# Performance work log

Hardware: AMD Instinct MI355X
Metric: run time of the kernel (lower is better)

The kernel has to match this reference:

```python
import jax, jax.numpy as jnp
import numpy as np

N_NODES = 100000
N_EDGES = 3200000
OUT_FEATURES = 128


def setup_inputs() -> dict:
    key = jax.random.key(0)
    k1, k2, k3, k4, k5 = jax.random.split(key, 5)
    edge_row = jax.random.randint(k1, (N_EDGES,), 0, N_NODES, dtype=jnp.int32)
    edge_col = jax.random.randint(k2, (N_EDGES,), 0, N_NODES, dtype=jnp.int32)
    edge_val = jax.random.uniform(k3, (N_EDGES,), dtype=jnp.float32)
    stdv = 1.0 / np.sqrt(OUT_FEATURES)
    weight = jax.random.uniform(k4, (N_NODES, OUT_FEATURES), minval=-stdv, maxval=stdv, dtype=jnp.float32)
    bias = jax.random.uniform(k5, (OUT_FEATURES,), minval=-stdv, maxval=stdv, dtype=jnp.float32)
    return {"edge_row": edge_row, "edge_col": edge_col, "edge_val": edge_val,
            "weight": weight, "bias": bias}


def reference(edge_row, edge_col, edge_val, weight, bias):
    # SpMM: out = adj @ weight, adj given in COO (row, col, val), shape [N, N]
    n_nodes = weight.shape[0]
    gathered = edge_val[:, None] * weight[edge_col]            # [E, F]
    out = jax.ops.segment_sum(gathered, edge_row, num_segments=n_nodes)  # [N, F]
    return out + bias
```

## Files before the change

kernel.cpp:

```cpp
#include <hip/hip_runtime.h>

#define F 128
#define RB 64
#define RB_SHIFT 6
#define CAP 4096
#define SCH 4096
#define PT3 512
#define EPT3 (SCH / PT3)
#define NSEG 8
#define COL_BITS 17
#define COL_MASK 0x1FFFF
#define MAXNB 2048

__global__ __launch_bounds__(256) void cvt_kernel(const float2* __restrict__ w2,
                                                  ushort* __restrict__ wq,
                                                  float* __restrict__ scales,
                                                  int n_nodes) {
    int row = blockIdx.x * 4 + (threadIdx.x >> 6);
    if (row >= n_nodes) return;
    int lane = threadIdx.x & 63;
    float2 f = w2[(size_t)row * 64 + lane];
    float m = fmaxf(fabsf(f.x), fabsf(f.y));
    for (int off = 32; off; off >>= 1) m = fmaxf(m, __shfl_xor(m, off));
    float inv = m > 0.f ? 127.f / m : 0.f;
    int q0 = (int)rintf(f.x * inv);
    int q1 = (int)rintf(f.y * inv);
    wq[(size_t)row * 64 + lane] = (ushort)((q0 & 0xFF) | ((q1 & 0xFF) << 8));
    if (lane == 0) scales[row] = m * (1.f / 127.f);
}

__global__ __launch_bounds__(256) void chist_kernel(const int* __restrict__ rows,
                                                    int* __restrict__ cntmat,
                                                    int n_edges, int nb) {
    __shared__ int h[MAXNB];
    int c = blockIdx.x, t = threadIdx.x;
    for (int i = t; i < nb; i += 256) h[i] = 0;
    __syncthreads();
    int e0 = c * SCH, e1 = min(e0 + SCH, n_edges);
    for (int e = e0 + t; e < e1; e += 256) atomicAdd(&h[rows[e] >> RB_SHIFT], 1);
    __syncthreads();
    for (int i = t; i < nb; i += 256) cntmat[(size_t)c * nb + i] = h[i];
}

__global__ __launch_bounds__(256) void scanA_kernel(int* __restrict__ cntmat,
                                                    int* __restrict__ segsum,
                                                    int nb, int nchunks) {
    int b = blockIdx.x * 256 + threadIdx.x;
    if (b >= nb) return;
    int sg = blockIdx.y;
    int cps = (nchunks + NSEG - 1) / NSEG;
    int c0 = sg * cps, c1 = min(c0 + cps, nchunks);
    int run = 0;
#pragma unroll 4
    for (int c = c0; c < c1; c++) {
        int v = cntmat[(size_t)c * nb + b];
        cntmat[(size_t)c * nb + b] = run;
        run += v;
    }
    segsum[sg * nb + b] = run;
}

__global__ __launch_bounds__(256) void scanB_kernel(int* __restrict__ segsum,
                                                    int* __restrict__ counts, int nb) {
    int b = blockIdx.x * 256 + threadIdx.x;
    if (b >= nb) return;
    int run = 0;
#pragma unroll
    for (int s = 0; s < NSEG; s++) {
        int v = segsum[s * nb + b];
        segsum[s * nb + b] = run;
        run += v;
    }
    counts[b] = run;
}

__global__ void bscan_kernel(const int* __restrict__ counts, int* __restrict__ boffs,
                             int nb) {
    __shared__ int lds[1024];
    int t = threadIdx.x;
    int per = (nb + 1023) / 1024;
    int base = t * per;
    int s = 0;
    for (int i = 0; i < per; i++)
        if (base + i < nb) s += counts[base + i];
    lds[t] = s;
    __syncthreads();
    for (int off = 1; off < 1024; off <<= 1) {
        int a = (t >= off) ? lds[t - off] : 0;
        __syncthreads();
        lds[t] += a;
        __syncthreads();
    }
    int excl = lds[t] - s;
    for (int i = 0; i < per; i++) {
        if (base + i < nb) {
            boffs[base + i] = excl;
            excl += counts[base + i];
        }
    }
    if (t == 1023) boffs[nb] = lds[1023];
}

__global__ __launch_bounds__(PT3) void scatter_kernel(
    const int* __restrict__ rows, const int* __restrict__ cols,
    const float* __restrict__ vals, const float* __restrict__ scales,
    const int* __restrict__ boffs, const int* __restrict__ segsum,
    const int* __restrict__ cntmat, int2* __restrict__ epk, int n_edges, int nb,
    int nchunks) {
    __shared__ int relc[MAXNB];
    __shared__ int hist[MAXNB];
    __shared__ int lcur[MAXNB];
    __shared__ int2 buf[SCH];
    __shared__ int sidx[SCH];
    int c = blockIdx.x;
    int t = threadIdx.x;
    int e0 = c * SCH, e1 = min(e0 + SCH, n_edges);
    int cnt = e1 - e0;
    int cps = (nchunks + NSEG - 1) / NSEG;
    int sg = c / cps;

    for (int i = t; i < nb; i += PT3) {
        relc[i] = boffs[i] + segsum[sg * nb + i] + cntmat[(size_t)c * nb + i];
        hist[i] = 0;
    }
    __syncthreads();

    int er[EPT3], ec[EPT3];
    float ev[EPT3];
#pragma unroll
    for (int k = 0; k < EPT3; k++) {
        int e = e0 + t + k * PT3;
        if (e < e1) {
            er[k] = rows[e];
            ec[k] = cols[e];
            ev[k] = vals[e] * scales[ec[k]];
            atomicAdd(&hist[er[k] >> RB_SHIFT], 1);
        }
    }
    __syncthreads();

    int b0 = t << 2;
    int h0 = (b0 + 0 < nb) ? hist[b0 + 0] : 0;
    int h1 = (b0 + 1 < nb) ? hist[b0 + 1] : 0;
    int h2 = (b0 + 2 < nb) ? hist[b0 + 2] : 0;
    int h3 = (b0 + 3 < nb) ? hist[b0 + 3] : 0;
    int psum = h0 + h1 + h2 + h3;
    int* temp = sidx;
    temp[t] = psum;
    __syncthreads();
    for (int off = 1; off < PT3; off <<= 1) {
        int a = (t >= off) ? temp[t - off] : 0;
        __syncthreads();
        temp[t] += a;
        __syncthreads();
    }
    int excl = temp[t] - psum;
    if (b0 + 0 < nb) { lcur[b0 + 0] = excl; relc[b0 + 0] -= excl; }
    excl += h0;
    if (b0 + 1 < nb) { lcur[b0 + 1] = excl; relc[b0 + 1] -= excl; }
    excl += h1;
    if (b0 + 2 < nb) { lcur[b0 + 2] = excl; relc[b0 + 2] -= excl; }
    excl += h2;
    if (b0 + 3 < nb) { lcur[b0 + 3] = excl; relc[b0 + 3] -= excl; }
    __syncthreads();

#pragma unroll
    for (int k = 0; k < EPT3; k++) {
        int e = e0 + t + k * PT3;
        if (e < e1) {
            int b = er[k] >> RB_SHIFT;
            int p = atomicAdd(&lcur[b], 1);
            buf[p] = make_int2(ec[k] | ((er[k] & (RB - 1)) << COL_BITS),
                               __float_as_int(ev[k]));
            sidx[p] = relc[b] + p;
        }
    }
    __syncthreads();

    for (int i = t; i < cnt; i += PT3) epk[sidx[i]] = buf[i];
}

__global__ __launch_bounds__(512, 8) void sortacc_kernel(
    const int* __restrict__ boffs, const int2* __restrict__ epk,
    const ushort* __restrict__ wq, const float* __restrict__ bias,
    float* __restrict__ out, int n_nodes) {
    __shared__ int2 buf[CAP];
    __shared__ int hist[RB], lstart[RB], lcur[RB];
    int b = blockIdx.x;
    int s = boffs[b];
    int cnt = boffs[b + 1] - s;
    int row0 = b << RB_SHIFT;
    int t = threadIdx.x;
    int lane = t & 63, w = t >> 6;
    float2 bb = ((const float2*)bias)[lane];

#define DEQX(u) ((float)(int)(signed char)((u) & 0xFF))
#define DEQY(u) ((float)(int)(signed char)((u) >> 8))

    if (cnt <= CAP) {
        if (t < RB) hist[t] = 0;
        __syncthreads();
        int2 r0, r1, r2, r3, r4, r5, r6, r7;
#define LOADK(rk, k)                                                     \
        {                                                                \
            int i = t + (k)*512;                                         \
            if (i < cnt) {                                               \
                rk = epk[s + i];                                         \
                atomicAdd(&hist[(unsigned)rk.x >> COL_BITS], 1);         \
            }                                                            \
        }
        LOADK(r0, 0) LOADK(r1, 1) LOADK(r2, 2) LOADK(r3, 3)
        LOADK(r4, 4) LOADK(r5, 5) LOADK(r6, 6) LOADK(r7, 7)
#undef LOADK
        __syncthreads();
        if (t < RB) lstart[t] = hist[t];
        __syncthreads();
        for (int off = 1; off < RB; off <<= 1) {
            int a = 0;
            if (t < RB && t >= off) a = lstart[t - off];
            __syncthreads();
            if (t < RB) lstart[t] += a;
            __syncthreads();
        }
        if (t < RB) {
            int st = lstart[t] - hist[t];
            lstart[t] = st;
            lcur[t] = st;
        }
        __syncthreads();
#define SCATK(rk, k)                                                     \
        {                                                                \
            int i = t + (k)*512;                                         \
            if (i < cnt) {                                               \
                int p = atomicAdd(&lcur[(unsigned)rk.x >> COL_BITS], 1); \
                buf[p] = rk;                                             \
            }                                                            \
        }
        SCATK(r0, 0) SCATK(r1, 1) SCATK(r2, 2) SCATK(r3, 3)
        SCATK(r4, 4) SCATK(r5, 5) SCATK(r6, 6) SCATK(r7, 7)
#undef SCATK
        __syncthreads();

        for (int j = 0; j < 8; j++) {
            int rl = w * 8 + j;
            int gr = row0 + rl;
            if (gr >= n_nodes) break;
            int e = lstart[rl];
            int end = e + hist[rl];
            float ax = 0.f, ay = 0.f;
            for (; e + 8 <= end; e += 8) {
                int2 p0 = buf[e], p1 = buf[e + 1], p2 = buf[e + 2], p3 = buf[e + 3];
                int2 p4 = buf[e + 4], p5 = buf[e + 5], p6 = buf[e + 6], p7 = buf[e + 7];
                uint u0 = wq[((size_t)(p0.x & COL_MASK) << 6) + lane];
                uint u1 = wq[((size_t)(p1.x & COL_MASK) << 6) + lane];
                uint u2 = wq[((size_t)(p2.x & COL_MASK) << 6) + lane];
                uint u3 = wq[((size_t)(p3.x & COL_MASK) << 6) + lane];
                uint u4 = wq[((size_t)(p4.x & COL_MASK) << 6) + lane];
                uint u5 = wq[((size_t)(p5.x & COL_MASK) << 6) + lane];
                uint u6 = wq[((size_t)(p6.x & COL_MASK) << 6) + lane];
                uint u7 = wq[((size_t)(p7.x & COL_MASK) << 6) + lane];
                float v0 = __int_as_float(p0.y), v1 = __int_as_float(p1.y);
                float v2 = __int_as_float(p2.y), v3 = __int_as_float(p3.y);
                float v4 = __int_as_float(p4.y), v5 = __int_as_float(p5.y);
                float v6 = __int_as_float(p6.y), v7 = __int_as_float(p7.y);
                ax += v0 * DEQX(u0) + v1 * DEQX(u1) + v2 * DEQX(u2) + v3 * DEQX(u3) +
                      v4 * DEQX(u4) + v5 * DEQX(u5) + v6 * DEQX(u6) + v7 * DEQX(u7);
                ay += v0 * DEQY(u0) + v1 * DEQY(u1) + v2 * DEQY(u2) + v3 * DEQY(u3) +
                      v4 * DEQY(u4) + v5 * DEQY(u5) + v6 * DEQY(u6) + v7 * DEQY(u7);
            }
            for (; e < end; ++e) {
                int2 pk = buf[e];
                uint u = wq[((size_t)(pk.x & COL_MASK) << 6) + lane];
                float v = __int_as_float(pk.y);
                ax += v * DEQX(u);
                ay += v * DEQY(u);
            }
            ((float2*)(out + (size_t)gr * F))[lane] = make_float2(ax + bb.x, ay + bb.y);
        }
    } else {
        for (int j = 0; j < 8; j++) {
            int rl = w * 8 + j;
            int gr = row0 + rl;
            if (gr >= n_nodes) break;
            float ax = 0.f, ay = 0.f;
            for (int e = s; e < s + cnt; ++e) {
                int2 pk = epk[e];
                if ((int)((unsigned)pk.x >> COL_BITS) == rl) {
                    uint u = wq[((size_t)(pk.x & COL_MASK) << 6) + lane];
                    float v = __int_as_float(pk.y);
                    ax += v * DEQX(u);
                    ay += v * DEQY(u);
                }
            }
            ((float2*)(out + (size_t)gr * F))[lane] = make_float2(ax + bb.x, ay + bb.y);
        }
    }
#undef DEQX
#undef DEQY
}

__global__ void init_out_kernel(float* __restrict__ out, const float* __restrict__ bias,
                                int n_nodes) {
    const float4* b4 = (const float4*)bias;
    float4* o4 = (float4*)out;
    int total = n_nodes * (F / 4);
    for (int i = blockIdx.x * blockDim.x + threadIdx.x; i < total;
         i += gridDim.x * blockDim.x)
        o4[i] = b4[i & (F / 4 - 1)];
}

__global__ void edge_scatter_kernel(const int* __restrict__ rows,
                                    const int* __restrict__ cols,
                                    const float* __restrict__ vals,
                                    const float* __restrict__ weight,
                                    float* __restrict__ out, int n_edges) {
    int e = (blockIdx.x * blockDim.x + threadIdx.x) >> 6;
    if (e >= n_edges) return;
    int lane = threadIdx.x & 63;
    float2 w = ((const float2*)(weight + (size_t)cols[e] * F))[lane];
    float val = vals[e];
    float* o = out + (size_t)rows[e] * F + lane * 2;
    unsafeAtomicAdd(o, val * w.x);
    unsafeAtomicAdd(o + 1, val * w.y);
}

extern "C" void kernel_launch(void* const* d_in, const int* in_sizes, int n_in,
                              void* d_out, int out_size, void* d_ws, size_t ws_size,
                              hipStream_t stream) {
    const int*   rows   = (const int*)d_in[0];
    const int*   cols   = (const int*)d_in[1];
    const float* vals   = (const float*)d_in[2];
    const float* weight = (const float*)d_in[3];
    const float* bias   = (const float*)d_in[4];
    float* out = (float*)d_out;

    int n_edges = in_sizes[0];
    int n_nodes = out_size / F;
    int nb = (n_nodes + RB - 1) / RB;
    int nchunks = (n_edges + SCH - 1) / SCH;

    size_t head_ints  = ((size_t)2 * nb + 2) & ~(size_t)1;
    size_t epk_off    = head_ints * 4;
    size_t scales_off = epk_off + (size_t)n_edges * 8;
    size_t wq_off     = (scales_off + (size_t)n_nodes * 4 + 255) & ~(size_t)255;
    size_t mat_off    = (wq_off + (size_t)n_nodes * F + 255) & ~(size_t)255;
    size_t seg_off    = mat_off + (size_t)nchunks * nb * 4;
    size_t need       = seg_off + (size_t)NSEG * nb * 4;

    if (ws_size < need || n_nodes > (1 << COL_BITS) || nb > MAXNB) {
        init_out_kernel<<<2048, 256, 0, stream>>>(out, bias, n_nodes);
        int grid = (n_edges + 3) / 4;
        edge_scatter_kernel<<<grid, 256, 0, stream>>>(rows, cols, vals, weight, out,
                                                      n_edges);
        return;
    }

    int* counts   = (int*)d_ws;
    int* boffs    = counts + nb;
    int2* epk     = (int2*)((char*)d_ws + epk_off);
    float* scales = (float*)((char*)d_ws + scales_off);
    ushort* wq    = (ushort*)((char*)d_ws + wq_off);
    int* cntmat   = (int*)((char*)d_ws + mat_off);
    int* segsum   = (int*)((char*)d_ws + seg_off);

    cvt_kernel<<<(n_nodes + 3) / 4, 256, 0, stream>>>((const float2*)weight, wq, scales,
                                                      n_nodes);
    chist_kernel<<<nchunks, 256, 0, stream>>>(rows, cntmat, n_edges, nb);
    dim3 ga((nb + 255) / 256, NSEG);
    scanA_kernel<<<ga, 256, 0, stream>>>(cntmat, segsum, nb, nchunks);
    scanB_kernel<<<(nb + 255) / 256, 256, 0, stream>>>(segsum, counts, nb);
    bscan_kernel<<<1, 1024, 0, stream>>>(counts, boffs, nb);
    scatter_kernel<<<nchunks, PT3, 0, stream>>>(rows, cols, vals, scales, boffs, segsum,
                                                cntmat, epk, n_edges, nb, nchunks);
    sortacc_kernel<<<nb, 512, 0, stream>>>(boffs, epk, wq, bias, out, n_nodes);
}
```

Measured before the change: 168.5 us.

## Merge preprocessing kernels, use wave-shuffle scans, and make scatter/accumulate persistent

Fuses the weight-quantization and chunk-histogram kernels into one launch, and merges the second-level segment scan with the block-offset scan into a single kernel. The LDS-barrier prefix scans in scatter and sortacc are replaced with wave shuffle-up scans plus a small cross-wave step. Scatter and sortacc become grid-stride loops over capped grids. The aim is to cut launch count and barrier overhead, at the cost of extra per-iteration syncs and possible load imbalance from the capped grids. scanBC handles at most two buckets per thread, which is enough for nb up to 2048.

```diff
diff --git a/kernel.cpp b/kernel.cpp
--- a/kernel.cpp
+++ b/kernel.cpp
@@ -11,35 +11,35 @@
 #define COL_BITS 17
 #define COL_MASK 0x1FFFF
 #define MAXNB 2048
-
-__global__ __launch_bounds__(256) void cvt_kernel(const float2* __restrict__ w2,
-                                                  ushort* __restrict__ wq,
-                                                  float* __restrict__ scales,
-                                                  int n_nodes) {
-    int row = blockIdx.x * 4 + (threadIdx.x >> 6);
-    if (row >= n_nodes) return;
-    int lane = threadIdx.x & 63;
-    float2 f = w2[(size_t)row * 64 + lane];
-    float m = fmaxf(fabsf(f.x), fabsf(f.y));
-    for (int off = 32; off; off >>= 1) m = fmaxf(m, __shfl_xor(m, off));
-    float inv = m > 0.f ? 127.f / m : 0.f;
-    int q0 = (int)rintf(f.x * inv);
-    int q1 = (int)rintf(f.y * inv);
-    wq[(size_t)row * 64 + lane] = (ushort)((q0 & 0xFF) | ((q1 & 0xFF) << 8));
-    if (lane == 0) scales[row] = m * (1.f / 127.f);
-}
-
-__global__ __launch_bounds__(256) void chist_kernel(const int* __restrict__ rows,
-                                                    int* __restrict__ cntmat,
-                                                    int n_edges, int nb) {
-    __shared__ int h[MAXNB];
-    int c = blockIdx.x, t = threadIdx.x;
-    for (int i = t; i < nb; i += 256) h[i] = 0;
-    __syncthreads();
-    int e0 = c * SCH, e1 = min(e0 + SCH, n_edges);
-    for (int e = e0 + t; e < e1; e += 256) atomicAdd(&h[rows[e] >> RB_SHIFT], 1);
-    __syncthreads();
-    for (int i = t; i < nb; i += 256) cntmat[(size_t)c * nb + i] = h[i];
+#define PGRID 512
+#define SGRID 1024
+
+__global__ __launch_bounds__(256) void cvt_chist_kernel(
+    const float2* __restrict__ w2, ushort* __restrict__ wq, float* __restrict__ scales,
+    int n_nodes, const int* __restrict__ rows, int* __restrict__ cntmat, int n_edges,
+    int nb, int nchunks) {
+    if ((int)blockIdx.x < nchunks) {
+        __shared__ int h[MAXNB];
+        int c = blockIdx.x, t = threadIdx.x;
+        for (int i = t; i < nb; i += 256) h[i] = 0;
+        __syncthreads();
+        int e0 = c * SCH, e1 = min(e0 + SCH, n_edges);
+        for (int e = e0 + t; e < e1; e += 256) atomicAdd(&h[rows[e] >> RB_SHIFT], 1);
+        __syncthreads();
+        for (int i = t; i < nb; i += 256) cntmat[(size_t)c * nb + i] = h[i];
+    } else {
+        int row = (blockIdx.x - nchunks) * 4 + (threadIdx.x >> 6);
+        if (row >= n_nodes) return;
+        int lane = threadIdx.x & 63;
+        float2 f = w2[(size_t)row * 64 + lane];
+        float m = fmaxf(fabsf(f.x), fabsf(f.y));
+        for (int off = 32; off; off >>= 1) m = fmaxf(m, __shfl_xor(m, off));
+        float inv = m > 0.f ? 127.f / m : 0.f;
+        int q0 = (int)rintf(f.x * inv);
+        int q1 = (int)rintf(f.y * inv);
+        wq[(size_t)row * 64 + lane] = (ushort)((q0 & 0xFF) | ((q1 & 0xFF) << 8));
+        if (lane == 0) scales[row] = m * (1.f / 127.f);
+    }
 }
 
 __global__ __launch_bounds__(256) void scanA_kernel(int* __restrict__ cntmat,
@@ -60,29 +60,26 @@
     segsum[sg * nb + b] = run;
 }
 
-__global__ __launch_bounds__(256) void scanB_kernel(int* __restrict__ segsum,
-                                                    int* __restrict__ counts, int nb) {
-    int b = blockIdx.x * 256 + threadIdx.x;
-    if (b >= nb) return;
-    int run = 0;
-#pragma unroll
-    for (int s = 0; s < NSEG; s++) {
-        int v = segsum[s * nb + b];
-        segsum[s * nb + b] = run;
-        run += v;
-    }
-    counts[b] = run;
-}
-
-__global__ void bscan_kernel(const int* __restrict__ counts, int* __restrict__ boffs,
-                             int nb) {
+__global__ void scanBC_kernel(int* __restrict__ segsum, int* __restrict__ boffs, int nb) {
     __shared__ int lds[1024];
     int t = threadIdx.x;
     int per = (nb + 1023) / 1024;
     int base = t * per;
+    int cnt[2] = {0, 0};
     int s = 0;
-    for (int i = 0; i < per; i++)
-        if (base + i < nb) s += counts[base + i];
+    for (int i = 0; i < per && i < 2; i++) {
+        int b = base + i;
+        int run = 0;
+        if (b < nb) {
+            for (int sg = 0; sg < NSEG; sg++) {
+                int v = segsum[sg * nb + b];
+                segsum[sg * nb + b] = run;
+                run += v;
+            }
+        }
+        cnt[i] = run;
+        s += run;
+    }
     lds[t] = s;
     __syncthreads();
     for (int off = 1; off < 1024; off <<= 1) {
@@ -92,10 +89,11 @@
         __syncthreads();
     }
     int excl = lds[t] - s;
-    for (int i = 0; i < per; i++) {
-        if (base + i < nb) {
-            boffs[base + i] = excl;
-            excl += counts[base + i];
+    for (int i = 0; i < per && i < 2; i++) {
+        int b = base + i;
+        if (b < nb) {
+            boffs[b] = excl;
+            excl += cnt[i];
         }
     }
     if (t == 1023) boffs[nb] = lds[1023];
@@ -112,84 +110,92 @@
     __shared__ int lcur[MAXNB];
     __shared__ int2 buf[SCH];
     __shared__ int sidx[SCH];
-    int c = blockIdx.x;
+    __shared__ int wsum[PT3 / 64], wbase[PT3 / 64];
     int t = threadIdx.x;
-    int e0 = c * SCH, e1 = min(e0 + SCH, n_edges);
-    int cnt = e1 - e0;
+    int lane = t & 63, w = t >> 6;
     int cps = (nchunks + NSEG - 1) / NSEG;
-    int sg = c / cps;
-
-    for (int i = t; i < nb; i += PT3) {
-        relc[i] = boffs[i] + segsum[sg * nb + i] + cntmat[(size_t)c * nb + i];
-        hist[i] = 0;
-    }
-    __syncthreads();
-
-    int er[EPT3], ec[EPT3];
-    float ev[EPT3];
+
+    for (int c = blockIdx.x; c < nchunks; c += gridDim.x) {
+        int e0 = c * SCH, e1 = min(e0 + SCH, n_edges);
+        int cnt = e1 - e0;
+        int sg = c / cps;
+
+        for (int i = t; i < nb; i += PT3) {
+            relc[i] = boffs[i] + segsum[sg * nb + i] + cntmat[(size_t)c * nb + i];
+            hist[i] = 0;
+        }
+        __syncthreads();
+
+        int er[EPT3], ec[EPT3];
+        float ev[EPT3];
 #pragma unroll
-    for (int k = 0; k < EPT3; k++) {
-        int e = e0 + t + k * PT3;
-        if (e < e1) {
-            er[k] = rows[e];
-            ec[k] = cols[e];
-            ev[k] = vals[e] * scales[ec[k]];
-            atomicAdd(&hist[er[k] >> RB_SHIFT], 1);
-        }
-    }
-    __syncthreads();
-
-    int b0 = t << 2;
-    int h0 = (b0 + 0 < nb) ? hist[b0 + 0] : 0;
-    int h1 = (b0 + 1 < nb) ? hist[b0 + 1] : 0;
-    int h2 = (b0 + 2 < nb) ? hist[b0 + 2] : 0;
-    int h3 = (b0 + 3 < nb) ? hist[b0 + 3] : 0;
-    int psum = h0 + h1 + h2 + h3;
-    int* temp = sidx;
-    temp[t] = psum;
-    __syncthreads();
-    for (int off = 1; off < PT3; off <<= 1) {
-        int a = (t >= off) ? temp[t - off] : 0;
-        __syncthreads();
-        temp[t] += a;
-        __syncthreads();
-    }
-    int excl = temp[t] - psum;
-    if (b0 + 0 < nb) { lcur[b0 + 0] = excl; relc[b0 + 0] -= excl; }
-    excl += h0;
-    if (b0 + 1 < nb) { lcur[b0 + 1] = excl; relc[b0 + 1] -= excl; }
-    excl += h1;
-    if (b0 + 2 < nb) { lcur[b0 + 2] = excl; relc[b0 + 2] -= excl; }
-    excl += h2;
-    if (b0 + 3 < nb) { lcur[b0 + 3] = excl; relc[b0 + 3] -= excl; }
-    __syncthreads();
-
+        for (int k = 0; k < EPT3; k++) {
+            int e = e0 + t + k * PT3;
+            if (e < e1) {
+                er[k] = rows[e];
+                ec[k] = cols[e];
+                ev[k] = vals[e] * scales[ec[k]];
+                atomicAdd(&hist[er[k] >> RB_SHIFT], 1);
+            }
+        }
+        __syncthreads();
+
+        int b0 = t << 2;
+        int h0 = (b0 + 0 < nb) ? hist[b0 + 0] : 0;
+        int h1 = (b0 + 1 < nb) ? hist[b0 + 1] : 0;
+        int h2 = (b0 + 2 < nb) ? hist[b0 + 2] : 0;
+        int h3 = (b0 + 3 < nb) ? hist[b0 + 3] : 0;
+        int psum = h0 + h1 + h2 + h3;
+        int v = psum;
 #pragma unroll
-    for (int k = 0; k < EPT3; k++) {
-        int e = e0 + t + k * PT3;
-        if (e < e1) {
-            int b = er[k] >> RB_SHIFT;
-            int p = atomicAdd(&lcur[b], 1);
-            buf[p] = make_int2(ec[k] | ((er[k] & (RB - 1)) << COL_BITS),
-                               __float_as_int(ev[k]));
-            sidx[p] = relc[b] + p;
-        }
-    }
-    __syncthreads();
-
-    for (int i = t; i < cnt; i += PT3) epk[sidx[i]] = buf[i];
+        for (int off = 1; off < 64; off <<= 1) {
+            int a = __shfl_up(v, off);
+            if (lane >= off) v += a;
+        }
+        if (lane == 63) wsum[w] = v;
+        __syncthreads();
+        if (t == 0) {
+            int run = 0;
+            for (int i = 0; i < PT3 / 64; i++) {
+                wbase[i] = run;
+                run += wsum[i];
+            }
+        }
+        __syncthreads();
+        int excl = v - psum + wbase[w];
+        if (b0 + 0 < nb) { lcur[b0 + 0] = excl; relc[b0 + 0] -= excl; }
+        excl += h0;
+        if (b0 + 1 < nb) { lcur[b0 + 1] = excl; relc[b0 + 1] -= excl; }
+        excl += h1;
+        if (b0 + 2 < nb) { lcur[b0 + 2] = excl; relc[b0 + 2] -= excl; }
+        excl += h2;
+        if (b0 + 3 < nb) { lcur[b0 + 3] = excl; relc[b0 + 3] -= excl; }
+        __syncthreads();
+
+#pragma unroll
+        for (int k = 0; k < EPT3; k++) {
+            int e = e0 + t + k * PT3;
+            if (e < e1) {
+                int b = er[k] >> RB_SHIFT;
+                int p = atomicAdd(&lcur[b], 1);
+                buf[p] = make_int2(ec[k] | ((er[k] & (RB - 1)) << COL_BITS),
+                                   __float_as_int(ev[k]));
+                sidx[p] = relc[b] + p;
+            }
+        }
+        __syncthreads();
+
+        for (int i = t; i < cnt; i += PT3) epk[sidx[i]] = buf[i];
+        __syncthreads();
+    }
 }
 
 __global__ __launch_bounds__(512, 8) void sortacc_kernel(
     const int* __restrict__ boffs, const int2* __restrict__ epk,
     const ushort* __restrict__ wq, const float* __restrict__ bias,
-    float* __restrict__ out, int n_nodes) {
+    float* __restrict__ out, int n_nodes, int nb) {
     __shared__ int2 buf[CAP];
     __shared__ int hist[RB], lstart[RB], lcur[RB];
-    int b = blockIdx.x;
-    int s = boffs[b];
-    int cnt = boffs[b + 1] - s;
-    int row0 = b << RB_SHIFT;
     int t = threadIdx.x;
     int lane = t & 63, w = t >> 6;
     float2 bb = ((const float2*)bias)[lane];
@@ -197,103 +203,107 @@
 #define DEQX(u) ((float)(int)(signed char)((u) & 0xFF))
 #define DEQY(u) ((float)(int)(signed char)((u) >> 8))
 
-    if (cnt <= CAP) {
-        if (t < RB) hist[t] = 0;
-        __syncthreads();
-        int2 r0, r1, r2, r3, r4, r5, r6, r7;
+    for (int b = blockIdx.x; b < nb; b += gridDim.x) {
+        int s = boffs[b];
+        int cnt = boffs[b + 1] - s;
+        int row0 = b << RB_SHIFT;
+
+        if (cnt <= CAP) {
+            if (t < RB) hist[t] = 0;
+            __syncthreads();
+            int2 r0, r1, r2, r3, r4, r5, r6, r7;
 #define LOADK(rk, k)                                                     \
-        {                                                                \
-            int i = t + (k)*512;                                         \
-            if (i < cnt) {                                               \
-                rk = epk[s + i];                                         \
-                atomicAdd(&hist[(unsigned)rk.x >> COL_BITS], 1);         \
-            }                                                            \
-        }
-        LOADK(r0, 0) LOADK(r1, 1) LOADK(r2, 2) LOADK(r3, 3)
-        LOADK(r4, 4) LOADK(r5, 5) LOADK(r6, 6) LOADK(r7, 7)
+            {                                                            \
+                int i = t + (k)*512;                                     \
+                if (i < cnt) {                                           \
+                    rk = epk[s + i];                                     \
+                    atomicAdd(&hist[(unsigned)rk.x >> COL_BITS], 1);     \
+                }                                                        \
+            }
+            LOADK(r0, 0) LOADK(r1, 1) LOADK(r2, 2) LOADK(r3, 3)
+            LOADK(r4, 4) LOADK(r5, 5) LOADK(r6, 6) LOADK(r7, 7)
 #undef LOADK
-        __syncthreads();
-        if (t < RB) lstart[t] = hist[t];
-        __syncthreads();
-        for (int off = 1; off < RB; off <<= 1) {
-            int a = 0;
-            if (t < RB && t >= off) a = lstart[t - off];
             __syncthreads();
-            if (t < RB) lstart[t] += a;
+            if (w == 0) {
+                int hv = hist[lane];
+                int v = hv;
+#pragma unroll
+                for (int off = 1; off < 64; off <<= 1) {
+                    int a = __shfl_up(v, off);
+                    if (lane >= off) v += a;
+                }
+                lstart[lane] = v - hv;
+                lcur[lane] = v - hv;
+            }
             __syncthreads();
-        }
-        if (t < RB) {
-            int st = lstart[t] - hist[t];
-            lstart[t] = st;
-            lcur[t] = st;
-        }
-        __syncthreads();
-#define SCATK(rk, k)                                                     \
-        {                                                                \
-            int i = t + (k)*512;                                         \
-            if (i < cnt) {                                               \
-                int p = atomicAdd(&lcur[(unsigned)rk.x >> COL_BITS], 1); \
-                buf[p] = rk;                                             \
-            }                                                            \
-        }
-        SCATK(r0, 0) SCATK(r1, 1) SCATK(r2, 2) SCATK(r3, 3)
-        SCATK(r4, 4) SCATK(r5, 5) SCATK(r6, 6) SCATK(r7, 7)
+#define SCATK(rk, k)                                                         \
+            {                                                                \
+                int i = t + (k)*512;                                         \
+                if (i < cnt) {                                               \
+                    int p = atomicAdd(&lcur[(unsigned)rk.x >> COL_BITS], 1); \
+                    buf[p] = rk;                                             \
+                }                                                            \
+            }
+            SCATK(r0, 0) SCATK(r1, 1) SCATK(r2, 2) SCATK(r3, 3)
+            SCATK(r4, 4) SCATK(r5, 5) SCATK(r6, 6) SCATK(r7, 7)
 #undef SCATK
-        __syncthreads();
-
-        for (int j = 0; j < 8; j++) {
-            int rl = w * 8 + j;
-            int gr = row0 + rl;
-            if (gr >= n_nodes) break;
-            int e = lstart[rl];
-            int end = e + hist[rl];
-            float ax = 0.f, ay = 0.f;
-            for (; e + 8 <= end; e += 8) {
-                int2 p0 = buf[e], p1 = buf[e + 1], p2 = buf[e + 2], p3 = buf[e + 3];
-                int2 p4 = buf[e + 4], p5 = buf[e + 5], p6 = buf[e + 6], p7 = buf[e + 7];
-                uint u0 = wq[((size_t)(p0.x & COL_MASK) << 6) + lane];
-                uint u1 = wq[((size_t)(p1.x & COL_MASK) << 6) + lane];
-                uint u2 = wq[((size_t)(p2.x & COL_MASK) << 6) + lane];
-                uint u3 = wq[((size_t)(p3.x & COL_MASK) << 6) + lane];
-                uint u4 = wq[((size_t)(p4.x & COL_MASK) << 6) + lane];
-                uint u5 = wq[((size_t)(p5.x & COL_MASK) << 6) + lane];
-                uint u6 = wq[((size_t)(p6.x & COL_MASK) << 6) + lane];
-                uint u7 = wq[((size_t)(p7.x & COL_MASK) << 6) + lane];
-                float v0 = __int_as_float(p0.y), v1 = __int_as_float(p1.y);
-                float v2 = __int_as_float(p2.y), v3 = __int_as_float(p3.y);
-                float v4 = __int_as_float(p4.y), v5 = __int_as_float(p5.y);
-                float v6 = __int_as_float(p6.y), v7 = __int_as_float(p7.y);
-                ax += v0 * DEQX(u0) + v1 * DEQX(u1) + v2 * DEQX(u2) + v3 * DEQX(u3) +
-                      v4 * DEQX(u4) + v5 * DEQX(u5) + v6 * DEQX(u6) + v7 * DEQX(u7);
-                ay += v0 * DEQY(u0) + v1 * DEQY(u1) + v2 * DEQY(u2) + v3 * DEQY(u3) +
-                      v4 * DEQY(u4) + v5 * DEQY(u5) + v6 * DEQY(u6) + v7 * DEQY(u7);
-            }
-            for (; e < end; ++e) {
-                int2 pk = buf[e];
-                uint u = wq[((size_t)(pk.x & COL_MASK) << 6) + lane];
-                float v = __int_as_float(pk.y);
-                ax += v * DEQX(u);
-                ay += v * DEQY(u);
-            }
-            ((float2*)(out + (size_t)gr * F))[lane] = make_float2(ax + bb.x, ay + bb.y);
-        }
-    } else {
-        for (int j = 0; j < 8; j++) {
-            int rl = w * 8 + j;
-            int gr = row0 + rl;
-            if (gr >= n_nodes) break;
-            float ax = 0.f, ay = 0.f;
-            for (int e = s; e < s + cnt; ++e) {
-                int2 pk = epk[e];
-                if ((int)((unsigned)pk.x >> COL_BITS) == rl) {
+            __syncthreads();
+
+            for (int j = 0; j < 8; j++) {
+                int rl = w * 8 + j;
+                int gr = row0 + rl;
+                if (gr >= n_nodes) break;
+                int e = lstart[rl];
+                int end = e + hist[rl];
+                float ax = 0.f, ay = 0.f;
+                for (; e + 8 <= end; e += 8) {
+                    int2 p0 = buf[e], p1 = buf[e + 1], p2 = buf[e + 2], p3 = buf[e + 3];
+                    int2 p4 = buf[e + 4], p5 = buf[e + 5], p6 = buf[e + 6], p7 = buf[e + 7];
+                    uint u0 = wq[((size_t)(p0.x & COL_MASK) << 6) + lane];
+                    uint u1 = wq[((size_t)(p1.x & COL_MASK) << 6) + lane];
+                    uint u2 = wq[((size_t)(p2.x & COL_MASK) << 6) + lane];
+                    uint u3 = wq[((size_t)(p3.x & COL_MASK) << 6) + lane];
+                    uint u4 = wq[((size_t)(p4.x & COL_MASK) << 6) + lane];
+                    uint u5 = wq[((size_t)(p5.x & COL_MASK) << 6) + lane];
+                    uint u6 = wq[((size_t)(p6.x & COL_MASK) << 6) + lane];
+                    uint u7 = wq[((size_t)(p7.x & COL_MASK) << 6) + lane];
+                    float v0 = __int_as_float(p0.y), v1 = __int_as_float(p1.y);
+                    float v2 = __int_as_float(p2.y), v3 = __int_as_float(p3.y);
+                    float v4 = __int_as_float(p4.y), v5 = __int_as_float(p5.y);
+                    float v6 = __int_as_float(p6.y), v7 = __int_as_float(p7.y);
+                    ax += v0 * DEQX(u0) + v1 * DEQX(u1) + v2 * DEQX(u2) + v3 * DEQX(u3) +
+                          v4 * DEQX(u4) + v5 * DEQX(u5) + v6 * DEQX(u6) + v7 * DEQX(u7);
+                    ay += v0 * DEQY(u0) + v1 * DEQY(u1) + v2 * DEQY(u2) + v3 * DEQY(u3) +
+                          v4 * DEQY(u4) + v5 * DEQY(u5) + v6 * DEQY(u6) + v7 * DEQY(u7);
+                }
+                for (; e < end; ++e) {
+                    int2 pk = buf[e];
                     uint u = wq[((size_t)(pk.x & COL_MASK) << 6) + lane];
                     float v = __int_as_float(pk.y);
                     ax += v * DEQX(u);
                     ay += v * DEQY(u);
                 }
-            }
-            ((float2*)(out + (size_t)gr * F))[lane] = make_float2(ax + bb.x, ay + bb.y);
-        }
+                ((float2*)(out + (size_t)gr * F))[lane] = make_float2(ax + bb.x, ay + bb.y);
+            }
+        } else {
+            for (int j = 0; j < 8; j++) {
+                int rl = w * 8 + j;
+                int gr = row0 + rl;
+                if (gr >= n_nodes) break;
+                float ax = 0.f, ay = 0.f;
+                for (int e = s; e < s + cnt; ++e) {
+                    int2 pk = epk[e];
+                    if ((int)((unsigned)pk.x >> COL_BITS) == rl) {
+                        uint u = wq[((size_t)(pk.x & COL_MASK) << 6) + lane];
+                        float v = __int_as_float(pk.y);
+                        ax += v * DEQX(u);
+                        ay += v * DEQY(u);
+                    }
+                }
+                ((float2*)(out + (size_t)gr * F))[lane] = make_float2(ax + bb.x, ay + bb.y);
+            }
+        }
+        __syncthreads();
     }
 #undef DEQX
 #undef DEQY
@@ -339,7 +349,7 @@
     int nb = (n_nodes + RB - 1) / RB;
     int nchunks = (n_edges + SCH - 1) / SCH;
 
-    size_t head_ints  = ((size_t)2 * nb + 2) & ~(size_t)1;
+    size_t head_ints  = ((size_t)nb + 2) & ~(size_t)1;
     size_t epk_off    = head_ints * 4;
     size_t scales_off = epk_off + (size_t)n_edges * 8;
     size_t wq_off     = (scales_off + (size_t)n_nodes * 4 + 255) & ~(size_t)255;
@@ -355,22 +365,21 @@
         return;
     }
 
-    int* counts   = (int*)d_ws;
-    int* boffs    = counts + nb;
+    int* boffs    = (int*)d_ws;
     int2* epk     = (int2*)((char*)d_ws + epk_off);
     float* scales = (float*)((char*)d_ws + scales_off);
     ushort* wq    = (ushort*)((char*)d_ws + wq_off);
     int* cntmat   = (int*)((char*)d_ws + mat_off);
     int* segsum   = (int*)((char*)d_ws + seg_off);
 
-    cvt_kernel<<<(n_nodes + 3) / 4, 256, 0, stream>>>((const float2*)weight, wq, scales,
-                                                      n_nodes);
-    chist_kernel<<<nchunks, 256, 0, stream>>>(rows, cntmat, n_edges, nb);
+    int cvt_blocks = (n_nodes + 3) / 4;
+    cvt_chist_kernel<<<nchunks + cvt_blocks, 256, 0, stream>>>(
+        (const float2*)weight, wq, scales, n_nodes, rows, cntmat, n_edges, nb, nchunks);
     dim3 ga((nb + 255) / 256, NSEG);
     scanA_kernel<<<ga, 256, 0, stream>>>(cntmat, segsum, nb, nchunks);
-    scanB_kernel<<<(nb + 255) / 256, 256, 0, stream>>>(segsum, counts, nb);
-    bscan_kernel<<<1, 1024, 0, stream>>>(counts, boffs, nb);
-    scatter_kernel<<<nchunks, PT3, 0, stream>>>(rows, cols, vals, scales, boffs, segsum,
-                                                cntmat, epk, n_edges, nb, nchunks);
-    sortacc_kernel<<<nb, 512, 0, stream>>>(boffs, epk, wq, bias, out, n_nodes);
-}
+    scanBC_kernel<<<1, 1024, 0, stream>>>(segsum, boffs, nb);
+    scatter_kernel<<<min(nchunks, PGRID), PT3, 0, stream>>>(
+        rows, cols, vals, scales, boffs, segsum, cntmat, epk, n_edges, nb, nchunks);
+    sortacc_kernel<<<min(nb, SGRID), 512, 0, stream>>>(boffs, epk, wq, bias, out,
+                                                       n_nodes, nb);
+}
```

Result: slower. 180.4 us (+7.0%).
